# Performance work log

Hardware: AMD Instinct MI355X
Metric: run time of the kernel (lower is better)

## Reference

```python
import jax, jax.numpy as jnp
import numpy as np

N = 65536        # query points per chunk
V = 512          # latent shape vertices
K = 8            # cdist top-k
H = 512          # hidden dim
NB = 4           # num blocks
NL = 2           # extra hidden layers per block
F0 = (V + 1) * 3 + 3 * K   # 1563 first-block input features
FI = F0 + H                # 2075 later-block input features (skip concat)


def setup_inputs() -> dict:
    key = jax.random.key(0)
    ks = jax.random.split(key, 6)
    s = 0.02  # small weight scale to keep tanh unsaturated
    return {
        "cxyz": jax.random.normal(ks[0], (N, 3 + 3 * V), dtype=jnp.float32),
        "W_first": jax.random.normal(ks[1], (F0, H), dtype=jnp.float32) * s,
        "b_first": jnp.zeros((H,), jnp.float32),
        "W_in": jax.random.normal(ks[2], (NB - 1, FI, H), dtype=jnp.float32) * s,
        "b_in": jnp.zeros((NB - 1, H), jnp.float32),
        "W_hidden": jax.random.normal(ks[3], (NB, NL, H, H), dtype=jnp.float32) * s,
        "b_hidden": jnp.zeros((NB, NL, H), jnp.float32),
        "W_out": jax.random.normal(ks[4], (H, 1), dtype=jnp.float32) * s,
        "b_out": jnp.zeros((1,), jnp.float32),
    }


def _forward(cxyz, W_first, b_first, W_in, b_in, W_hidden, b_hidden, W_out, b_out):
    xyz = cxyz[:, :3]                       # [N, 3]
    latent = cxyz[:, 3:]                    # [N, 3V]
    lat3 = latent.reshape(latent.shape[0], -1, 3)  # [N, V, 3]

    # kNN retrieval: squared euclidean distances give identical top-k indices
    # to torch.cdist (sqrt is monotone); we only use the indices.
    d2 = jnp.sum((xyz[:, None, :] - lat3) ** 2, axis=-1)   # [N, V]
    _, idx = jax.lax.top_k(-d2, K)                          # smallest-K indices [N, K]
    sel = jnp.take_along_axis(lat3, idx[:, :, None], axis=1)  # [N, K, 3]

    xyz_aug = jnp.concatenate([xyz, sel.reshape(sel.shape[0], -1)], axis=1)  # [N, 3+3K]
    x_ = jnp.concatenate([xyz_aug, latent], axis=1)                          # [N, F0]

    relu = jax.nn.relu
    # block 0
    x = relu(x_ @ W_first + b_first)
    for l in range(NL):
        x = relu(x @ W_hidden[0, l] + b_hidden[0, l])
    # blocks 1..NB-1 with skip concat of x_
    for b in range(1, NB):
        x = jnp.concatenate([x, x_], axis=1)   # [N, FI]
        x = relu(x @ W_in[b - 1] + b_in[b - 1])
        for l in range(NL):
            x = relu(x @ W_hidden[b, l] + b_hidden[b, l])
    return jnp.tanh(x @ W_out + b_out)          # [N, 1]


def reference(cxyz, W_first, b_first, W_in, b_in, W_hidden, b_hidden, W_out, b_out):
    return _forward(cxyz, W_first, b_first, W_in, b_in, W_hidden, b_hidden, W_out, b_out)
```

## Files before the change

kernel.cpp:

```cpp
#include <hip/hip_runtime.h>

typedef unsigned short u16;
typedef _Float16 f16;
typedef __attribute__((ext_vector_type(8))) _Float16 f16x8;
typedef __attribute__((ext_vector_type(4))) float f32x4;

#define NPTS 65536

__device__ __forceinline__ u16 f2h(float f) {
    f16 h = (f16)f;
    return __builtin_bit_cast(u16, h);
}

__device__ __forceinline__ unsigned pack2(float a, float b) {
    return (unsigned)f2h(a) | ((unsigned)f2h(b) << 16);
}

__device__ __forceinline__ void async_copy16(const u16* g, u16* l) {
    __builtin_amdgcn_global_load_lds(
        (const __attribute__((address_space(1))) void*)g,
        (__attribute__((address_space(3))) void*)l, 16, 0, 0);
}

__global__ __launch_bounds__(256) void knn_kernel(const float* __restrict__ cxyz,
                                                  u16* __restrict__ xpad) {
#pragma clang fp contract(off)
    const int lane = threadIdx.x & 63;
    const int wave = threadIdx.x >> 6;
    const size_t p = (size_t)blockIdx.x * 4 + wave;
    const float* row = cxyz + p * 1539;
    u16* orow = xpad + p * 1568;

    float vals[24];
    const float* lp = row + 3 + lane * 24;
#pragma unroll
    for (int i = 0; i < 24; ++i) vals[i] = lp[i];

    float x0 = row[0], y0 = row[1], z0 = row[2];

    unsigned long long cand[8];
#pragma unroll
    for (int t = 0; t < 8; ++t) {
        float dx = x0 - vals[3 * t + 0];
        float dy = y0 - vals[3 * t + 1];
        float dz = z0 - vals[3 * t + 2];
        float d2 = dx * dx + dy * dy;
        d2 = d2 + dz * dz;
        cand[t] = (((unsigned long long)__float_as_uint(d2)) << 32) |
                  (unsigned)(lane * 8 + t);
    }

    for (int r = 0; r < 8; ++r) {
        unsigned long long m = cand[0];
#pragma unroll
        for (int t = 1; t < 8; ++t) m = (cand[t] < m) ? cand[t] : m;
#pragma unroll
        for (int o = 1; o < 64; o <<= 1) {
            unsigned long long o2 = __shfl_xor(m, o, 64);
            m = (o2 < m) ? o2 : m;
        }
#pragma unroll
        for (int t = 0; t < 8; ++t)
            if (cand[t] == m) cand[t] = ~0ULL;
        if (lane == r) {
            unsigned jw = (unsigned)m;
            orow[3 + 3 * r + 0] = f2h(row[3 + 3 * jw + 0]);
            orow[3 + 3 * r + 1] = f2h(row[3 + 3 * jw + 1]);
            orow[3 + 3 * r + 2] = f2h(row[3 + 3 * jw + 2]);
        }
    }

    if (lane < 3) orow[lane] = f2h(row[lane]);
    if (lane >= 27 && lane < 32) orow[lane] = 0;

    unsigned w[12];
#pragma unroll
    for (int i = 0; i < 12; ++i) w[i] = pack2(vals[2 * i], vals[2 * i + 1]);
    uint4* op = (uint4*)(orow + 32 + lane * 24);
    op[0] = make_uint4(w[0], w[1], w[2], w[3]);
    op[1] = make_uint4(w[4], w[5], w[6], w[7]);
    op[2] = make_uint4(w[8], w[9], w[10], w[11]);
}

__global__ __launch_bounds__(256) void prep_w1(const float* __restrict__ Wf,
                                               u16* __restrict__ W1p) {
    int idx = blockIdx.x * 256 + threadIdx.x;
    if (idx >= 512 * 1568) return;
    int n = idx / 1568, kp = idx % 1568;
    float v = 0.f;
    if (kp < 27) v = Wf[(size_t)kp * 512 + n];
    else if (kp >= 32) v = Wf[(size_t)(kp - 5) * 512 + n];
    W1p[idx] = f2h(v);
}

__global__ __launch_bounds__(256) void prep_win(const float* __restrict__ Win,
                                                u16* __restrict__ Winp) {
    int idx = blockIdx.x * 256 + threadIdx.x;
    if (idx >= 3 * 512 * 2080) return;
    int b = idx / (512 * 2080);
    int r = idx % (512 * 2080);
    int n = r / 2080, kp = r % 2080;
    float v = 0.f;
    if (kp < 539) v = Win[((size_t)b * 2075 + kp) * 512 + n];
    else if (kp >= 544) v = Win[((size_t)b * 2075 + kp - 5) * 512 + n];
    Winp[idx] = f2h(v);
}

__global__ __launch_bounds__(256) void prep_wh(const float* __restrict__ Wh,
                                               u16* __restrict__ Whp) {
    int idx = blockIdx.x * 256 + threadIdx.x;
    if (idx >= 8 * 512 * 512) return;
    int m = idx / (512 * 512);
    int r = idx % (512 * 512);
    int n = r / 512, k = r % 512;
    Whp[idx] = f2h(Wh[((size_t)m * 512 + k) * 512 + n]);
}

__global__ __launch_bounds__(256) void gemm_f16(
    const u16* __restrict__ A0, int ld0, int kt0,
    const u16* __restrict__ A1, int ld1, int kt1,
    const u16* __restrict__ B,
    const float* __restrict__ bias,
    u16* __restrict__ C) {
    __shared__ u16 As[128 * 32];
    __shared__ u16 Bs[128 * 32];
    const int tid = threadIdx.x;
    const int lane = tid & 63;
    const int wave = tid >> 6;
    const int ktot = kt0 + kt1;
    const size_t ldB = (size_t)ktot * 32;
    const size_t mbase = (size_t)blockIdx.x * 128;
    const int nbase = blockIdx.y * 128;

    f32x4 acc[4][4];
#pragma unroll
    for (int i = 0; i < 4; ++i)
#pragma unroll
        for (int j = 0; j < 4; ++j) acc[i][j] = (f32x4){0.f, 0.f, 0.f, 0.f};

    const int r4 = lane >> 2;
    const int c8 = (lane & 3) * 8;
    u16* lA0 = &As[(wave * 32 + 0) * 32];
    u16* lA1 = &As[(wave * 32 + 16) * 32];
    u16* lB0 = &Bs[(wave * 32 + 0) * 32];
    u16* lB1 = &Bs[(wave * 32 + 16) * 32];
    const size_t arow0 = mbase + wave * 32 + r4;
    const size_t brow0 = (size_t)nbase + wave * 32 + r4;

    const int m0 = (wave & 1) * 64;
    const int n0 = (wave >> 1) * 64;
    const int rowsel = lane & 15;
    const int quad8 = (lane >> 4) * 8;

    for (int t = 0; t < ktot; ++t) {
        if (t < kt0) {
            const size_t off = arow0 * (size_t)ld0 + t * 32 + c8;
            async_copy16(A0 + off, lA0);
            async_copy16(A0 + off + 16 * (size_t)ld0, lA1);
        } else {
            const size_t off = arow0 * (size_t)ld1 + (t - kt0) * 32 + c8;
            async_copy16(A1 + off, lA0);
            async_copy16(A1 + off + 16 * (size_t)ld1, lA1);
        }
        {
            const size_t off = brow0 * ldB + t * 32 + c8;
            async_copy16(B + off, lB0);
            async_copy16(B + off + 16 * ldB, lB1);
        }
        __syncthreads();

        f16x8 af[4], bfr[4];
#pragma unroll
        for (int i = 0; i < 4; ++i) {
            af[i]  = __builtin_bit_cast(f16x8, *(const uint4*)&As[(m0 + i * 16 + rowsel) * 32 + quad8]);
            bfr[i] = __builtin_bit_cast(f16x8, *(const uint4*)&Bs[(n0 + i * 16 + rowsel) * 32 + quad8]);
        }
#pragma unroll
        for (int i = 0; i < 4; ++i)
#pragma unroll
            for (int j = 0; j < 4; ++j)
                acc[i][j] = __builtin_amdgcn_mfma_f32_16x16x32_f16(
                    af[i], bfr[j], acc[i][j], 0, 0, 0);
        __syncthreads();
    }

#pragma unroll
    for (int j = 0; j < 4; ++j) {
        const int col = nbase + n0 + j * 16 + (lane & 15);
        const float bv = bias[col];
#pragma unroll
        for (int i = 0; i < 4; ++i) {
#pragma unroll
            for (int r = 0; r < 4; ++r) {
                const size_t rowg = mbase + m0 + i * 16 + (lane >> 4) * 4 + r;
                float v = acc[i][j][r] + bv;
                v = v > 0.f ? v : 0.f;
                C[rowg * 512 + col] = f2h(v);
            }
        }
    }
}

__global__ __launch_bounds__(256) void out_kernel(const u16* __restrict__ x,
                                                  const float* __restrict__ Wout,
                                                  const float* __restrict__ bout,
                                                  float* __restrict__ out) {
    const int lane = threadIdx.x & 63;
    const int wave = threadIdx.x >> 6;
    const size_t p = (size_t)blockIdx.x * 4 + wave;
    uint4 xv = *(const uint4*)(x + p * 512 + lane * 8);
    const f16* xs = (const f16*)&xv;
    float s = 0.f;
#pragma unroll
    for (int i = 0; i < 8; ++i) s += (float)xs[i] * Wout[lane * 8 + i];
#pragma unroll
    for (int o = 1; o < 64; o <<= 1) s += __shfl_xor(s, o, 64);
    if (lane == 0) out[p] = tanhf(s + bout[0]);
}

extern "C" void kernel_launch(void* const* d_in, const int* in_sizes, int n_in,
                              void* d_out, int out_size, void* d_ws, size_t ws_size,
                              hipStream_t stream) {
    const float* cxyz = (const float*)d_in[0];
    const float* Wf   = (const float*)d_in[1];
    const float* bf   = (const float*)d_in[2];
    const float* Win  = (const float*)d_in[3];
    const float* bin  = (const float*)d_in[4];
    const float* Wh   = (const float*)d_in[5];
    const float* bh   = (const float*)d_in[6];
    const float* Wout = (const float*)d_in[7];
    const float* bout = (const float*)d_in[8];
    float* out = (float*)d_out;
    u16* wsb = (u16*)d_ws;

    const size_t N = NPTS;
    u16* xpad = wsb;
    u16* xa   = xpad + N * 1568;
    u16* xb   = xa + N * 512;
    u16* W1p  = xb + N * 512;
    u16* Winp = W1p + (size_t)512 * 1568;
    u16* Whp  = Winp + (size_t)3 * 512 * 2080;

    knn_kernel<<<dim3(N / 4), dim3(256), 0, stream>>>(cxyz, xpad);

    prep_w1<<<dim3((512 * 1568 + 255) / 256), dim3(256), 0, stream>>>(Wf, W1p);
    prep_win<<<dim3((3 * 512 * 2080 + 255) / 256), dim3(256), 0, stream>>>(Win, Winp);
    prep_wh<<<dim3((8 * 512 * 512 + 255) / 256), dim3(256), 0, stream>>>(Wh, Whp);

    const dim3 gg(N / 128, 4), gb(256);
    const size_t WH = (size_t)512 * 512;
    const size_t WI = (size_t)512 * 2080;

    gemm_f16<<<gg, gb, 0, stream>>>(xpad, 1568, 49, nullptr, 0, 0, W1p, bf, xa);
    gemm_f16<<<gg, gb, 0, stream>>>(xa, 512, 16, nullptr, 0, 0, Whp + 0 * WH, bh + 0 * 512, xb);
    gemm_f16<<<gg, gb, 0, stream>>>(xb, 512, 16, nullptr, 0, 0, Whp + 1 * WH, bh + 1 * 512, xa);

    gemm_f16<<<gg, gb, 0, stream>>>(xa, 512, 16, xpad, 1568, 49, Winp + 0 * WI, bin + 0 * 512, xb);
    gemm_f16<<<gg, gb, 0, stream>>>(xb, 512, 16, nullptr, 0, 0, Whp + 2 * WH, bh + 2 * 512, xa);
    gemm_f16<<<gg, gb, 0, stream>>>(xa, 512, 16, nullptr, 0, 0, Whp + 3 * WH, bh + 3 * 512, xb);

    gemm_f16<<<gg, gb, 0, stream>>>(xb, 512, 16, xpad, 1568, 49, Winp + 1 * WI, bin + 1 * 512, xa);
    gemm_f16<<<gg, gb, 0, stream>>>(xa, 512, 16, nullptr, 0, 0, Whp + 4 * WH, bh + 4 * 512, xb);
    gemm_f16<<<gg, gb, 0, stream>>>(xb, 512, 16, nullptr, 0, 0, Whp + 5 * WH, bh + 5 * 512, xa);

    gemm_f16<<<gg, gb, 0, stream>>>(xa, 512, 16, xpad, 1568, 49, Winp + 2 * WI, bin + 2 * 512, xb);
    gemm_f16<<<gg, gb, 0, stream>>>(xb, 512, 16, nullptr, 0, 0, Whp + 6 * WH, bh + 6 * 512, xa);
    gemm_f16<<<gg, gb, 0, stream>>>(xa, 512, 16, nullptr, 0, 0, Whp + 7 * WH, bh + 7 * 512, xb);

    out_kernel<<<dim3(N / 4), dim3(256), 0, stream>>>(xb, Wout, bout, out);
}
```

Before: 2.163 ms.

## Double-buffer GEMM LDS tiles and remap blocks for XCD-aware L2 reuse

Measured after the change: 1.768 ms. 18.3% less time.

```diff
diff --git a/kernel.cpp b/kernel.cpp
--- a/kernel.cpp
+++ b/kernel.cpp
@@ -116,21 +116,27 @@
     Whp[idx] = f2h(Wh[((size_t)m * 512 + k) * 512 + n]);
 }
 
-__global__ __launch_bounds__(256) void gemm_f16(
+__global__ __launch_bounds__(256, 4) void gemm_f16(
     const u16* __restrict__ A0, int ld0, int kt0,
     const u16* __restrict__ A1, int ld1, int kt1,
     const u16* __restrict__ B,
     const float* __restrict__ bias,
-    u16* __restrict__ C) {
-    __shared__ u16 As[128 * 32];
-    __shared__ u16 Bs[128 * 32];
+    u16* __restrict__ C,
+    int mb8) {
+    __shared__ u16 As[2][128 * 32];
+    __shared__ u16 Bs[2][128 * 32];
     const int tid = threadIdx.x;
     const int lane = tid & 63;
     const int wave = tid >> 6;
     const int ktot = kt0 + kt1;
     const size_t ldB = (size_t)ktot * 32;
-    const size_t mbase = (size_t)blockIdx.x * 128;
-    const int nbase = blockIdx.y * 128;
+
+    const int bid = blockIdx.x;
+    const int idx = bid >> 3;
+    const int mb = (bid & 7) * mb8 + (idx >> 2);
+    const int nb = idx & 3;
+    const size_t mbase = (size_t)mb * 128;
+    const int nbase = nb * 128;
 
     f32x4 acc[4][4];
 #pragma unroll
@@ -140,10 +146,6 @@
 
     const int r4 = lane >> 2;
     const int c8 = (lane & 3) * 8;
-    u16* lA0 = &As[(wave * 32 + 0) * 32];
-    u16* lA1 = &As[(wave * 32 + 16) * 32];
-    u16* lB0 = &Bs[(wave * 32 + 0) * 32];
-    u16* lB1 = &Bs[(wave * 32 + 16) * 32];
     const size_t arow0 = mbase + wave * 32 + r4;
     const size_t brow0 = (size_t)nbase + wave * 32 + r4;
 
@@ -152,7 +154,11 @@
     const int rowsel = lane & 15;
     const int quad8 = (lane >> 4) * 8;
 
-    for (int t = 0; t < ktot; ++t) {
+    auto stage = [&](int t, int b) {
+        u16* lA0 = &As[b][(wave * 32 + 0) * 32];
+        u16* lA1 = &As[b][(wave * 32 + 16) * 32];
+        u16* lB0 = &Bs[b][(wave * 32 + 0) * 32];
+        u16* lB1 = &Bs[b][(wave * 32 + 16) * 32];
         if (t < kt0) {
             const size_t off = arow0 * (size_t)ld0 + t * 32 + c8;
             async_copy16(A0 + off, lA0);
@@ -162,18 +168,23 @@
             async_copy16(A1 + off, lA0);
             async_copy16(A1 + off + 16 * (size_t)ld1, lA1);
         }
-        {
-            const size_t off = brow0 * ldB + t * 32 + c8;
-            async_copy16(B + off, lB0);
-            async_copy16(B + off + 16 * ldB, lB1);
-        }
-        __syncthreads();
+        const size_t boff = brow0 * ldB + t * 32 + c8;
+        async_copy16(B + boff, lB0);
+        async_copy16(B + boff + 16 * ldB, lB1);
+    };
+
+    stage(0, 0);
+    __syncthreads();
+
+    int cur = 0;
+    for (int t = 0; t < ktot; ++t) {
+        if (t + 1 < ktot) stage(t + 1, cur ^ 1);
 
         f16x8 af[4], bfr[4];
 #pragma unroll
         for (int i = 0; i < 4; ++i) {
-            af[i]  = __builtin_bit_cast(f16x8, *(const uint4*)&As[(m0 + i * 16 + rowsel) * 32 + quad8]);
-            bfr[i] = __builtin_bit_cast(f16x8, *(const uint4*)&Bs[(n0 + i * 16 + rowsel) * 32 + quad8]);
+            af[i]  = __builtin_bit_cast(f16x8, *(const uint4*)&As[cur][(m0 + i * 16 + rowsel) * 32 + quad8]);
+            bfr[i] = __builtin_bit_cast(f16x8, *(const uint4*)&Bs[cur][(n0 + i * 16 + rowsel) * 32 + quad8]);
         }
 #pragma unroll
         for (int i = 0; i < 4; ++i)
@@ -181,7 +192,9 @@
             for (int j = 0; j < 4; ++j)
                 acc[i][j] = __builtin_amdgcn_mfma_f32_16x16x32_f16(
                     af[i], bfr[j], acc[i][j], 0, 0, 0);
+
         __syncthreads();
+        cur ^= 1;
     }
 
 #pragma unroll
@@ -247,25 +260,26 @@
     prep_win<<<dim3((3 * 512 * 2080 + 255) / 256), dim3(256), 0, stream>>>(Win, Winp);
     prep_wh<<<dim3((8 * 512 * 512 + 255) / 256), dim3(256), 0, stream>>>(Wh, Whp);
 
-    const dim3 gg(N / 128, 4), gb(256);
+    const int MB8 = (int)(N / 128) / 8;
+    const dim3 gg((N / 128) * 4), gb(256);
     const size_t WH = (size_t)512 * 512;
     const size_t WI = (size_t)512 * 2080;
 
-    gemm_f16<<<gg, gb, 0, stream>>>(xpad, 1568, 49, nullptr, 0, 0, W1p, bf, xa);
-    gemm_f16<<<gg, gb, 0, stream>>>(xa, 512, 16, nullptr, 0, 0, Whp + 0 * WH, bh + 0 * 512, xb);
-    gemm_f16<<<gg, gb, 0, stream>>>(xb, 512, 16, nullptr, 0, 0, Whp + 1 * WH, bh + 1 * 512, xa);
-
-    gemm_f16<<<gg, gb, 0, stream>>>(xa, 512, 16, xpad, 1568, 49, Winp + 0 * WI, bin + 0 * 512, xb);
-    gemm_f16<<<gg, gb, 0, stream>>>(xb, 512, 16, nullptr, 0, 0, Whp + 2 * WH, bh + 2 * 512, xa);
-    gemm_f16<<<gg, gb, 0, stream>>>(xa, 512, 16, nullptr, 0, 0, Whp + 3 * WH, bh + 3 * 512, xb);
-
-    gemm_f16<<<gg, gb, 0, stream>>>(xb, 512, 16, xpad, 1568, 49, Winp + 1 * WI, bin + 1 * 512, xa);
-    gemm_f16<<<gg, gb, 0, stream>>>(xa, 512, 16, nullptr, 0, 0, Whp + 4 * WH, bh + 4 * 512, xb);
-    gemm_f16<<<gg, gb, 0, stream>>>(xb, 512, 16, nullptr, 0, 0, Whp + 5 * WH, bh + 5 * 512, xa);
-
-    gemm_f16<<<gg, gb, 0, stream>>>(xa, 512, 16, xpad, 1568, 49, Winp + 2 * WI, bin + 2 * 512, xb);
-    gemm_f16<<<gg, gb, 0, stream>>>(xb, 512, 16, nullptr, 0, 0, Whp + 6 * WH, bh + 6 * 512, xa);
-    gemm_f16<<<gg, gb, 0, stream>>>(xa, 512, 16, nullptr, 0, 0, Whp + 7 * WH, bh + 7 * 512, xb);
+    gemm_f16<<<gg, gb, 0, stream>>>(xpad, 1568, 49, nullptr, 0, 0, W1p, bf, xa, MB8);
+    gemm_f16<<<gg, gb, 0, stream>>>(xa, 512, 16, nullptr, 0, 0, Whp + 0 * WH, bh + 0 * 512, xb, MB8);
+    gemm_f16<<<gg, gb, 0, stream>>>(xb, 512, 16, nullptr, 0, 0, Whp + 1 * WH, bh + 1 * 512, xa, MB8);
+
+    gemm_f16<<<gg, gb, 0, stream>>>(xa, 512, 16, xpad, 1568, 49, Winp + 0 * WI, bin + 0 * 512, xb, MB8);
+    gemm_f16<<<gg, gb, 0, stream>>>(xb, 512, 16, nullptr, 0, 0, Whp + 2 * WH, bh + 2 * 512, xa, MB8);
+    gemm_f16<<<gg, gb, 0, stream>>>(xa, 512, 16, nullptr, 0, 0, Whp + 3 * WH, bh + 3 * 512, xb, MB8);
+
+    gemm_f16<<<gg, gb, 0, stream>>>(xb, 512, 16, xpad, 1568, 49, Winp + 1 * WI, bin + 1 * 512, xa, MB8);
+    gemm_f16<<<gg, gb, 0, stream>>>(xa, 512, 16, nullptr, 0, 0, Whp + 4 * WH, bh + 4 * 512, xb, MB8);
+    gemm_f16<<<gg, gb, 0, stream>>>(xb, 512, 16, nullptr, 0, 0, Whp + 5 * WH, bh + 5 * 512, xa, MB8);
+
+    gemm_f16<<<gg, gb, 0, stream>>>(xa, 512, 16, xpad, 1568, 49, Winp + 2 * WI, bin + 2 * 512, xb, MB8);
+    gemm_f16<<<gg, gb, 0, stream>>>(xb, 512, 16, nullptr, 0, 0, Whp + 6 * WH, bh + 6 * 512, xa, MB8);
+    gemm_f16<<<gg, gb, 0, stream>>>(xa, 512, 16, nullptr, 0, 0, Whp + 7 * WH, bh + 7 * 512, xb, MB8);
 
     out_kernel<<<dim3(N / 4), dim3(256), 0, stream>>>(xb, Wout, bout, out);
 }
```
